# Performance work log

Measured on AMD Instinct MI355X. Metric: run time of the kernel, lower is better.

Reference implementation:

```python
import jax, jax.numpy as jnp
import numpy as np

B, S, H = 16, 384, 768
DK, ESS, WHOLE = 64, 6, 8
HEADER = WHOLE + 1
NL_RGAT = 2


def _sinusoidal_pos(seq_len, dim):
    pos = np.arange(seq_len)[:, None]
    j = np.arange(dim)[None, :]
    enc = pos / np.power(10000.0, 2 * (j // 2) / dim)
    sent = dim // 2
    out = np.zeros((seq_len, dim), dtype=np.float32)
    out[:, :sent] = np.sin(enc[:, 0::2])
    out[:, sent:] = np.cos(enc[:, 1::2])
    return jnp.asarray(out)[None, None]  # [1,1,S,dim]


def _rope(pos, x):
    sin, cos = jnp.split(pos, 2, axis=-1)
    sin_pos = jnp.stack([sin, sin], -1).reshape(pos.shape)
    cos_pos = jnp.stack([cos, cos], -1).reshape(pos.shape)
    rot = jnp.stack([-x[..., 1::2], x[..., 0::2]], -1).reshape(x.shape)
    return x * cos_pos + rot * sin_pos


def _mlp(x, rep_w, rep_b, sc_w, sc_b):
    return jax.nn.relu(x @ rep_w.T + rep_b) @ sc_w.T + sc_b


def _heads(y, mask, n_heads):
    b, s = y.shape[:2]
    return (y * mask).reshape(b, s, n_heads, DK).transpose(0, 2, 1, 3)


def _shaking(M, rows, cols):
    # M: [B,nH,S,S] -> [B,P,nH]; upper triangle (incl diag), row-major
    return M[:, :, rows, cols].transpose(0, 2, 1)


def _layernorm(x, eps=1e-5):
    m = x.mean(-1, keepdims=True)
    v = ((x - m) ** 2).mean(-1, keepdims=True)
    return (x - m) * jax.lax.rsqrt(v + eps)


def setup_inputs() -> dict:
    key = jax.random.key(0)
    ks = jax.random.split(key, 32)
    n = lambda i, shape: jax.random.normal(ks[i], shape, dtype=jnp.float32) * 0.02
    ig = (H + DK * HEADER) // 2          # 672
    ip = (2 * H + DK * ESS) // 2          # 960
    return dict(
        seq_hiddens=jax.random.normal(ks[0], (B, S, H), dtype=jnp.float32),
        attention_mask=jnp.ones((B, S, 1), dtype=jnp.float32),
        wq4gt_w=n(1, (DK, H)), wq4gt_b=n(2, (DK,)),
        wk4gt_w=n(3, (DK, H)), wk4gt_b=n(4, (DK,)),
        wq4g_rep_w=n(5, (ig, H)), wq4g_rep_b=n(6, (ig,)),
        wq4g_sc_w=n(7, (DK * HEADER, ig)), wq4g_sc_b=n(8, (DK * HEADER,)),
        wk4g_rep_w=n(9, (ig, H)), wk4g_rep_b=n(10, (ig,)),
        wk4g_sc_w=n(11, (DK * HEADER, ig)), wk4g_sc_b=n(12, (DK * HEADER,)),
        rgat_w=n(13, (NL_RGAT, HEADER, H, H)),
        wq4t_w=n(14, (DK, 2 * H)), wq4t_b=n(15, (DK,)),
        wk4t_w=n(16, (DK, 2 * H)), wk4t_b=n(17, (DK,)),
        wq_rep_w=n(18, (ip, 2 * H)), wq_rep_b=n(19, (ip,)),
        wq_sc_w=n(20, (DK * ESS, ip)), wq_sc_b=n(21, (DK * ESS,)),
        wk_rep_w=n(22, (ip, 2 * H)), wk_rep_b=n(23, (ip,)),
        wk_sc_w=n(24, (DK * ESS, ip)), wk_sc_b=n(25, (DK * ESS,)),
    )


def reference(seq_hiddens, attention_mask,
              wq4gt_w, wq4gt_b, wk4gt_w, wk4gt_b,
              wq4g_rep_w, wq4g_rep_b, wq4g_sc_w, wq4g_sc_b,
              wk4g_rep_w, wk4g_rep_b, wk4g_sc_w, wk4g_sc_b,
              rgat_w,
              wq4t_w, wq4t_b, wk4t_w, wk4t_b,
              wq_rep_w, wq_rep_b, wq_sc_w, wq_sc_b,
              wk_rep_w, wk_rep_b, wk_sc_w, wk_sc_b):
    pos = _sinusoidal_pos(S, DK)
    rows, cols = np.triu_indices(S)
    inv = 1.0 / np.sqrt(DK).astype(np.float32)
    mask = attention_mask
    x = seq_hiddens

    # ----- graph layer (graph_stack_num = 1) -----
    tsq = _rope(pos, _heads(x @ wq4gt_w.T + wq4gt_b, mask, 1))
    tsk = _rope(pos, _heads(x @ wk4gt_w.T + wk4gt_b, mask, 1))
    thr_g = jax.nn.relu(_shaking(jnp.einsum('bhqd,bhkd->bhqk', tsq, tsk) * inv, rows, cols))

    q = _rope(pos, _heads(_mlp(x, wq4g_rep_w, wq4g_rep_b, wq4g_sc_w, wq4g_sc_b), mask, HEADER))
    k = _rope(pos, _heads(_mlp(x, wk4g_rep_w, wk4g_rep_b, wk4g_sc_w, wk4g_sc_b), mask, HEADER))
    score = jnp.einsum('bhqd,bhkd->bhqk', q, k) * inv  # [B,HEADER,S,S]
    sc_g = _shaking(score[:, :WHOLE], rows, cols)

    upper = jnp.triu(score, 1)
    diag = jnp.triu(score, 0) - upper
    att = upper + jnp.swapaxes(upper, -1, -2) + diag  # symmetric
    adj = jax.nn.softmax(att, -1) * (att != 0)

    feat = x
    for l in range(NL_RGAT):
        hr = jnp.einsum('bsh,roh->brso', feat, rgat_w[l])           # per-relation Linear (no bias)
        agg = jax.nn.relu(jnp.einsum('brst,brto->brso', adj, hr))   # adjacency bmm + ReLU
        feat = _layernorm(jax.nn.relu(agg.sum(1)) / HEADER)         # (dropout is eval-identity)

    # ----- prediction head -----
    inp = jnp.concatenate([seq_hiddens, feat], -1)  # [B,S,2H]
    tq = _rope(pos, _heads(inp @ wq4t_w.T + wq4t_b, mask, 1))
    tk = _rope(pos, _heads(inp @ wk4t_w.T + wk4t_b, mask, 1))
    thr_p = jax.nn.relu(_shaking(jnp.einsum('bhqd,bhkd->bhqk', tq, tk) * inv, rows, cols))

    qp = _rope(pos, _heads(_mlp(inp, wq_rep_w, wq_rep_b, wq_sc_w, wq_sc_b), mask, ESS))
    kp = _rope(pos, _heads(_mlp(inp, wk_rep_w, wk_rep_b, wk_sc_w, wk_sc_b), mask, ESS))
    sc_p = _shaking(jnp.einsum('bhqd,bhkd->bhqk', qp, kp) * inv, rows, cols)

    # concat all shaking outputs along last dim: [B, S(S+1)/2, ESS+1+WHOLE+1]
    return jnp.concatenate([sc_p, thr_p, sc_g, thr_g], -1)
```

## Files before the change

### kernel.cpp

```cpp
#include <hip/hip_runtime.h>
#include <math.h>

typedef unsigned short ushort_t;
typedef __attribute__((ext_vector_type(8))) short short8;
typedef __attribute__((ext_vector_type(4))) float f32x4;

constexpr int B = 16, S = 384, H = 768;
constexpr int BS = B * S;
constexpr long long PAIRS = (long long)S * (S + 1) / 2;
constexpr float INV = 0.125f;

__device__ __forceinline__ ushort_t f2bf(float f) {
  unsigned int u = __float_as_uint(f);
  u += 0x7FFF + ((u >> 16) & 1);
  return (ushort_t)(u >> 16);
}
__device__ __forceinline__ float bf2f(ushort_t u) {
  return __uint_as_float(((unsigned int)u) << 16);
}

__device__ __forceinline__ void glds16(const ushort_t* g, ushort_t* l) {
  __builtin_amdgcn_global_load_lds(
      (const __attribute__((address_space(1))) unsigned int*)g,
      (__attribute__((address_space(3))) unsigned int*)l, 16, 0, 0);
}

__global__ __launch_bounds__(256) void setup_kernel(
    float* tab,
    const float* g_repq, const float* g_repk, const float* g_gtq, const float* g_gtk,
    const float* p_repq, const float* p_repk, const float* p_gtq, const float* p_gtk,
    const float* g_scq, const float* g_sck, const float* p_scq, const float* p_sck,
    float* bqkg, float* bqkp, float* bscg, float* bscp) {
  int b = blockIdx.x;
  if (b < 48) {
    int s = b * 8 + (threadIdx.x >> 5);
    int i = threadIdx.x & 31;
    double ang = (double)s / pow(10000.0, (double)i / 32.0);
    tab[s * 64 + 2 * i]     = (float)cos(ang);
    tab[s * 64 + 2 * i + 1] = (float)sin(ang);
  } else {
    int t = (b - 48) * 256 + threadIdx.x;
    if (t < 1472)
      bqkg[t] = t < 672 ? g_repq[t] : t < 1344 ? g_repk[t - 672]
              : t < 1408 ? g_gtq[t - 1344] : g_gtk[t - 1408];
    if (t < 2048)
      bqkp[t] = t < 960 ? p_repq[t] : t < 1920 ? p_repk[t - 960]
              : t < 1984 ? p_gtq[t - 1920] : p_gtk[t - 1984];
    if (t < 1152) bscg[t] = t < 576 ? g_scq[t] : g_sck[t - 576];
    if (t < 768)  bscp[t] = t < 384 ? p_scq[t] : p_sck[t - 384];
  }
}

constexpr int NJOBS = 14;
struct CvtJobs {
  const float* src[NJOBS];
  ushort_t* dst[NJOBS];
  int n_real[NJOBS];
  int n_tot[NJOBS];
  int blk_off[NJOBS + 1];
};
__global__ __launch_bounds__(256) void cvt_jobs_kernel(CvtJobs J) {
  int blk = blockIdx.x;
  int j = 0;
  while (j < NJOBS - 1 && blk >= J.blk_off[j + 1]) ++j;
  int i4 = (blk - J.blk_off[j]) * 256 + threadIdx.x;
  if (i4 * 4 >= J.n_tot[j]) return;
  ushort4 o;
  if (i4 * 4 < J.n_real[j]) {
    float4 v = ((const float4*)J.src[j])[i4];
    o = make_ushort4(f2bf(v.x), f2bf(v.y), f2bf(v.z), f2bf(v.w));
  } else {
    o = make_ushort4(0, 0, 0, 0);
  }
  ((ushort4*)J.dst[j])[i4] = o;
}

template <int ACT, int CMODE, int SWZ>
__global__ __launch_bounds__(256) void gemm_nt_mfma(
    const ushort_t* __restrict__ A, const ushort_t* __restrict__ W,
    const float* __restrict__ bias, void* __restrict__ Cv,
    ushort_t* __restrict__ pl, ushort_t* __restrict__ qd,
    ushort_t* __restrict__ kd, int cbase, int nsplit,
    int N, int K, int lda, int ldw, int ldc, float alpha, int nh,
    long long sAb, long long sAh, long long sWb, long long sWh,
    long long sCb, long long sCh,
    const float* __restrict__ mask, const float* __restrict__ tab, int biasN) {
  constexpr int SHSZ = (CMODE == 2 || CMODE == 8) ? 17408 : 16384;
  __shared__ __align__(16) ushort_t SH[SHSZ];
  int bx = blockIdx.x, by = blockIdx.y, bz = blockIdx.z;
  if (SWZ) {
    const int nx = gridDim.x, ny = gridDim.y;
    const int nwg = nx * ny * gridDim.z;
    const int hw = bx + nx * (by + ny * bz);
    int l = (hw & 7) * (nwg >> 3) + (hw >> 3);
    const int pz = l / (nx * ny);
    int l2 = l - pz * (nx * ny);
    const int GM = 8;
    const int band = l2 / (GM * nx);
    const int rem = l2 - band * (GM * nx);
    const int gm = (ny - band * GM < GM) ? (ny - band * GM) : GM;
    bx = rem / gm;
    by = band * GM + (rem - bx * gm);
    bz = pz;
  }
  const int zb = bz / nh, zh = bz - zb * nh;
  A += zb * sAb + zh * sAh;
  W += zb * sWb + zh * sWh;
  const int t = threadIdx.x;
  int m0, n0;
  if (CMODE == 3 || CMODE == 8) {
    const int ti = (bx < 3) ? 0 : (bx < 5 ? 1 : 2);
    const int tj = (bx < 3) ? bx : (bx < 5 ? bx - 2 : 2);
    m0 = ti * 128; n0 = tj * 128;
  } else {
    m0 = by * 128; n0 = bx * 128;
  }
  const int lane = t & 63, wid = t >> 6;
  const int wr = wid >> 1, wc = wid & 1;
  const int lrow = lane & 15, lk = lane >> 4;
  const int srow = t >> 2, sch = (t & 3) * 8;
  const ushort_t* Ag = A + (size_t)(m0 + srow) * lda + sch;
  const ushort_t* Wg = W + (size_t)(n0 + srow) * ldw + sch;
  const size_t a64 = (size_t)64 * lda, w64 = (size_t)64 * ldw;

  f32x4 acc[4][4];
#pragma unroll
  for (int i = 0; i < 4; ++i)
#pragma unroll
    for (int j = 0; j < 4; ++j) acc[i][j] = (f32x4){0.f, 0.f, 0.f, 0.f};

  auto stage = [&](int k0, int buf) {
    const int ao = buf * 4096, bo = 8192 + buf * 4096;
    glds16(Ag + k0, &SH[ao + t * 8]);
    glds16(Ag + k0 + a64, &SH[ao + 2048 + t * 8]);
    glds16(Wg + k0, &SH[bo + t * 8]);
    glds16(Wg + k0 + w64, &SH[bo + 2048 + t * 8]);
  };

  const int nk = K >> 5;
  stage(0, 0);
  for (int s = 0; s < nk; ++s) {
    __syncthreads();
    if (s + 1 < nk) stage((s + 1) << 5, (s + 1) & 1);
    const int ao = (s & 1) * 4096, bo = 8192 + (s & 1) * 4096;
    short8 av[4], bv[4];
#pragma unroll
    for (int i = 0; i < 4; ++i) {
      av[i] = *(const short8*)&SH[ao + (wr * 64 + i * 16 + lrow) * 32 + lk * 8];
      bv[i] = *(const short8*)&SH[bo + (wc * 64 + i * 16 + lrow) * 32 + lk * 8];
    }
#pragma unroll
    for (int i = 0; i < 4; ++i)
#pragma unroll
      for (int j = 0; j < 4; ++j)
        acc[i][j] = __builtin_amdgcn_mfma_f32_16x16x32_bf16(av[i], bv[j],
                                                            acc[i][j], 0, 0, 0);
  }

  if (CMODE == 2) {
    __syncthreads();
    const int bb = m0 / S;
    ushort_t* Cb = (ushort_t*)Cv + (size_t)bb * sCb;
    const int s_base = m0 - bb * S;
#pragma unroll
    for (int i = 0; i < 4; ++i) {
      const int sl = wr * 64 + i * 16 + lk * 4;
#pragma unroll
      for (int j = 0; j < 4; ++j) {
        const int nl = wc * 64 + j * 16 + lrow;
        ushort4 o = make_ushort4(f2bf(acc[i][j][0]), f2bf(acc[i][j][1]),
                                 f2bf(acc[i][j][2]), f2bf(acc[i][j][3]));
        *(ushort4*)&SH[nl * 136 + sl] = o;
      }
    }
    __syncthreads();
#pragma unroll
    for (int it = 0; it < 8; ++it) {
      const int row = it * 16 + wid * 4 + lk;
      ushort_t* dst = Cb + (size_t)(n0 + row) * ldc + s_base + lrow * 8;
      *(short8*)dst = *(const short8*)&SH[row * 136 + lrow * 8];
    }
  } else if (CMODE == 3) {
    ushort_t* plc = pl + ((size_t)(cbase + zh) * B + zb) * PAIRS;
#pragma unroll
    for (int j = 0; j < 4; ++j) {
      const int n = n0 + wc * 64 + j * 16 + lrow;
#pragma unroll
      for (int i = 0; i < 4; ++i) {
#pragma unroll
        for (int e = 0; e < 4; ++e) {
          const int m = m0 + wr * 64 + i * 16 + lk * 4 + e;
          if (n >= m) {
            long long p = (long long)m * S - (long long)m * (m - 1) / 2 + (n - m);
            float v = alpha * acc[i][j][e];
            if (ACT == 1) v = fmaxf(v, 0.f);
            plc[p] = f2bf(v);
          }
        }
      }
    }
  } else if (CMODE == 5) {
    ushort_t* Cq = qd + (size_t)zh * sCh;
    const float* bz2 = bias + (size_t)zh * biasN;
#pragma unroll
    for (int j = 0; j < 4; ++j) {
      const int n = n0 + wc * 64 + j * 16 + lrow;
      const float vb = (n < N) ? bz2[n] : 0.f;
      const int d = n & 63;
      const int ti2 = d & ~1;
#pragma unroll
      for (int i = 0; i < 4; ++i) {
#pragma unroll
        for (int e = 0; e < 4; ++e) {
          const int m = m0 + wr * 64 + i * 16 + lk * 4 + e;
          const int s = m % S;
          float v = (n < N) ? (acc[i][j][e] + vb) : 0.f;
          float pv = __shfl_xor(v, 1);
          float c = tab[s * 64 + ti2], sn = tab[s * 64 + ti2 + 1];
          float o = (d & 1) ? (v * c + pv * sn) : (v * c - pv * sn);
          o *= mask[m];
          if (n < N) Cq[(size_t)m * ldc + n] = f2bf(o);
        }
      }
    }
  } else if (CMODE == 6) {
    ushort_t* Cu = (ushort_t*)Cv;
#pragma unroll
    for (int j = 0; j < 4; ++j) {
      const int n = n0 + wc * 64 + j * 16 + lrow;
      const float vb = (n < N) ? bias[n] : 0.f;
#pragma unroll
      for (int i = 0; i < 4; ++i) {
#pragma unroll
        for (int e = 0; e < 4; ++e) {
          const int m = m0 + wr * 64 + i * 16 + lk * 4 + e;
          float v = (n < N) ? (acc[i][j][e] + vb) : 0.f;
          float pv = __shfl_xor(v, 1);
          if (n < nsplit) {
            Cu[(size_t)m * ldc + n] = f2bf(fmaxf(v, 0.f));
          } else if (n < N) {
            const int d = n - nsplit;
            const int dd = d & 63;
            const int ti2 = dd & ~1;
            const int s = m % S;
            float c = tab[s * 64 + ti2], sn = tab[s * 64 + ti2 + 1];
            float o = (dd & 1) ? (v * c + pv * sn) : (v * c - pv * sn);
            o *= mask[m];
            if (d < 64) qd[(size_t)m * 64 + dd] = f2bf(o);
            else        kd[(size_t)m * 64 + dd] = f2bf(o);
          }
        }
      }
    }
  } else if (CMODE == 8) {
    ushort_t* Cu = (ushort_t*)Cv + zb * sCb + zh * sCh;
    ushort_t* plc = pl + ((size_t)(cbase + zh) * B + zb) * PAIRS;
    const bool diag = (m0 == n0);
#pragma unroll
    for (int j = 0; j < 4; ++j) {
      const int n = n0 + wc * 64 + j * 16 + lrow;
#pragma unroll
      for (int i = 0; i < 4; ++i) {
#pragma unroll
        for (int e = 0; e < 4; ++e) {
          const int m = m0 + wr * 64 + i * 16 + lk * 4 + e;
          float v = alpha * acc[i][j][e];
          ushort_t vb = f2bf(v);
          if (!diag || n >= m) Cu[(size_t)m * ldc + n] = vb;
          if (zh < 8 && n >= m) {
            long long p = (long long)m * S - (long long)m * (m - 1) / 2 + (n - m);
            plc[p] = vb;
          }
        }
      }
    }
    __syncthreads();
#pragma unroll
    for (int i = 0; i < 4; ++i) {
      const int sl = wr * 64 + i * 16 + lk * 4;
#pragma unroll
      for (int j = 0; j < 4; ++j) {
        const int nl = wc * 64 + j * 16 + lrow;
        ushort4 o4 = make_ushort4(f2bf(alpha * acc[i][j][0]),
                                  f2bf(alpha * acc[i][j][1]),
                                  f2bf(alpha * acc[i][j][2]),
                                  f2bf(alpha * acc[i][j][3]));
        *(ushort4*)&SH[nl * 136 + sl] = o4;
      }
    }
    __syncthreads();
#pragma unroll
    for (int it = 0; it < 8; ++it) {
      const int rowN = it * 16 + wid * 4 + lk;
      const int colM = lrow * 8;
      if (!diag) {
        *(short8*)&Cu[(size_t)(n0 + rowN) * ldc + m0 + colM] =
            *(const short8*)&SH[rowN * 136 + colM];
      } else {
#pragma unroll
        for (int q = 0; q < 8; ++q)
          if (rowN > colM + q)
            Cu[(size_t)(n0 + rowN) * ldc + m0 + colM + q] =
                SH[rowN * 136 + colM + q];
      }
    }
  }
}

__global__ __launch_bounds__(256) void adj_bmm_kernel(
    const ushort_t* __restrict__ adjb, const ushort_t* __restrict__ hrt,
    float* __restrict__ P0, float* __restrict__ P1, float* __restrict__ P2) {
  __shared__ __align__(16) ushort_t As[2][128 * 32];
  __shared__ __align__(16) ushort_t Bs[2][128 * 32];
  int bx = blockIdx.x, by = blockIdx.y, bz = blockIdx.z;
  {
    int nx = gridDim.x, ny = gridDim.y;
    int nwg = nx * ny * gridDim.z;
    int flat = bx + nx * (by + ny * bz);
    int l = (flat & 7) * (nwg >> 3) + (flat >> 3);
    bx = l % nx; l /= nx; by = l % ny; bz = l / ny;
  }
  const int b = bz / 3, rg = bz - b * 3;
  float* P = (rg == 0) ? P0 : (rg == 1) ? P1 : P2;
  const int t = threadIdx.x;
  const int m0 = by * 128, n0 = bx * 128;
  const int lane = t & 63, wid = t >> 6;
  const int wr = wid >> 1, wc = wid & 1;
  const int lrow = lane & 15, lk = lane >> 4;
  const int srow = t >> 2, sch = (t & 3) * 8;

  const ushort_t* adjA =
      adjb + ((size_t)(b * 9 + rg * 3) * S + m0 + srow) * S + sch;
  const ushort_t* hrA =
      hrt + ((size_t)(b * 9 + rg * 3) * H + n0 + srow) * S + sch;

  float mac[4][4][4];
#pragma unroll
  for (int i = 0; i < 4; ++i)
#pragma unroll
    for (int j = 0; j < 4; ++j)
#pragma unroll
      for (int e = 0; e < 4; ++e) mac[i][j][e] = 0.f;

  f32x4 acc[4][4];
#pragma unroll
  for (int i = 0; i < 4; ++i)
#pragma unroll
    for (int j = 0; j < 4; ++j) acc[i][j] = (f32x4){0.f, 0.f, 0.f, 0.f};

  auto stage = [&](int s, int buf) {
    const int rr = s / 12;
    const int k0 = (s - rr * 12) * 32;
    const ushort_t* Ag = adjA + (size_t)rr * S * S + k0;
    const ushort_t* Wg = hrA + (size_t)rr * H * S + k0;
    glds16(Ag, &As[buf][t * 8]);
    glds16(Ag + 64 * S, &As[buf][2048 + t * 8]);
    glds16(Wg, &Bs[buf][t * 8]);
    glds16(Wg + 64 * S, &Bs[buf][2048 + t * 8]);
  };

  stage(0, 0);
  for (int s = 0; s < 36; ++s) {
    __syncthreads();
    if (s + 1 < 36) stage(s + 1, (s + 1) & 1);
    const int buf = s & 1;
    short8 av[4], bv[4];
#pragma unroll
    for (int i = 0; i < 4; ++i) {
      av[i] = *(const short8*)&As[buf][(wr * 64 + i * 16 + lrow) * 32 + lk * 8];
      bv[i] = *(const short8*)&Bs[buf][(wc * 64 + i * 16 + lrow) * 32 + lk * 8];
    }
#pragma unroll
    for (int i = 0; i < 4; ++i)
#pragma unroll
      for (int j = 0; j < 4; ++j)
        acc[i][j] = __builtin_amdgcn_mfma_f32_16x16x32_bf16(av[i], bv[j],
                                                            acc[i][j], 0, 0, 0);
    if ((s % 12) == 11) {
#pragma unroll
      for (int i = 0; i < 4; ++i)
#pragma unroll
        for (int j = 0; j < 4; ++j) {
#pragma unroll
          for (int e = 0; e < 4; ++e)
            mac[i][j][e] += fmaxf(acc[i][j][e], 0.f);
          acc[i][j] = (f32x4){0.f, 0.f, 0.f, 0.f};
        }
    }
  }

#pragma unroll
  for (int i = 0; i < 4; ++i)
#pragma unroll
    for (int j = 0; j < 4; ++j)
#pragma unroll
      for (int e = 0; e < 4; ++e) {
        const int m = m0 + wr * 64 + i * 16 + lk * 4 + e;
        const int n = n0 + wc * 64 + j * 16 + lrow;
        P[((size_t)b * S + m) * H + n] = mac[i][j][e];
      }
}

__global__ __launch_bounds__(128) void softmax_mask_kernel(
    const ushort_t* __restrict__ Mt, ushort_t* __restrict__ adjb) {
  __shared__ float red[128];
  int row = blockIdx.x;
  const ushort_t* r = Mt + (size_t)row * S;
  ushort_t* o = adjb + (size_t)row * S;
  int t = threadIdx.x;
  const bool act = t < 96;
  float v[4];
  float mx = -INFINITY;
  if (act) {
    ushort4 u = ((const ushort4*)r)[t];
    v[0] = bf2f(u.x); v[1] = bf2f(u.y); v[2] = bf2f(u.z); v[3] = bf2f(u.w);
    mx = fmaxf(fmaxf(v[0], v[1]), fmaxf(v[2], v[3]));
  }
  red[t] = mx; __syncthreads();
  for (int off2 = 64; off2 > 0; off2 >>= 1) {
    if (t < off2) red[t] = fmaxf(red[t], red[t + off2]);
    __syncthreads();
  }
  mx = red[0]; __syncthreads();
  float e4[4], s = 0.f;
  if (act) {
#pragma unroll
    for (int q = 0; q < 4; ++q) { e4[q] = expf(v[q] - mx); s += e4[q]; }
  }
  red[t] = s; __syncthreads();
  for (int off2 = 64; off2 > 0; off2 >>= 1) {
    if (t < off2) red[t] += red[t + off2];
    __syncthreads();
  }
  float invs = 1.f / red[0];
  if (act) {
    ushort4 ou;
    ou.x = f2bf((v[0] != 0.f) ? e4[0] * invs : 0.f);
    ou.y = f2bf((v[1] != 0.f) ? e4[1] * invs : 0.f);
    ou.z = f2bf((v[2] != 0.f) ? e4[2] * invs : 0.f);
    ou.w = f2bf((v[3] != 0.f) ? e4[3] * invs : 0.f);
    ((ushort4*)o)[t] = ou;
  }
}

__global__ __launch_bounds__(256) void ln_finalize_kernel(
    const float* __restrict__ P0, const float* __restrict__ P1,
    const float* __restrict__ P2, const ushort_t* __restrict__ xb,
    ushort_t* __restrict__ inp) {
  __shared__ float red[256];
  int row = blockIdx.x;
  const size_t base = (size_t)row * H;
  ushort_t* xrow = inp + (size_t)row * (2 * H);
  ushort_t* fb = xrow + H;
  int t = threadIdx.x;
  float v[3];
  float s = 0.f;
#pragma unroll
  for (int q = 0; q < 3; ++q) {
    size_t ix = base + t + q * 256;
    v[q] = (P0[ix] + P1[ix] + P2[ix]) / 9.0f;
    s += v[q];
  }
  red[t] = s; __syncthreads();
#pragma unroll
  for (int q = 0; q < 3; ++q)
    xrow[t + q * 256] = xb[base + t + q * 256];
  for (int off2 = 128; off2 > 0; off2 >>= 1) {
    if (t < off2) red[t] += red[t + off2];
    __syncthreads();
  }
  float mean = red[0] / (float)H; __syncthreads();
  float s2 = 0.f;
#pragma unroll
  for (int q = 0; q < 3; ++q) { float d = v[q] - mean; s2 += d * d; }
  red[t] = s2; __syncthreads();
  for (int off2 = 128; off2 > 0; off2 >>= 1) {
    if (t < off2) red[t] += red[t + off2];
    __syncthreads();
  }
  float var = red[0] / (float)H;
  float rs = rsqrtf(var + 1e-5f);
#pragma unroll
  for (int q = 0; q < 3; ++q)
    fb[t + q * 256] = f2bf((v[q] - mean) * rs);
}

__global__ __launch_bounds__(256) void gather16_kernel(
    const ushort_t* __restrict__ plA, const ushort_t* __restrict__ plB,
    float* __restrict__ out) {
  int idx = blockIdx.x * 256 + threadIdx.x;
  if (idx >= (int)(B * PAIRS)) return;
  const size_t PLN = (size_t)B * PAIRS;
  float v[16];
#pragma unroll
  for (int ch = 0; ch < 7; ++ch)  v[ch] = bf2f(plA[(size_t)ch * PLN + idx]);
#pragma unroll
  for (int ch = 7; ch < 16; ++ch) v[ch] = bf2f(plB[(size_t)(ch - 7) * PLN + idx]);
  float4* dst = (float4*)(out + (size_t)idx * 16);
#pragma unroll
  for (int q = 0; q < 4; ++q)
    dst[q] = make_float4(v[4 * q], v[4 * q + 1], v[4 * q + 2], v[4 * q + 3]);
}

extern "C" void kernel_launch(void* const* d_in, const int* in_sizes, int n_in,
                              void* d_out, int out_size, void* d_ws, size_t ws_size,
                              hipStream_t stream) {
  (void)in_sizes; (void)n_in; (void)out_size; (void)ws_size;
  const float* x          = (const float*)d_in[0];
  const float* mask       = (const float*)d_in[1];
  const float* wq4gt_w    = (const float*)d_in[2];
  const float* wq4gt_b    = (const float*)d_in[3];
  const float* wk4gt_w    = (const float*)d_in[4];
  const float* wk4gt_b    = (const float*)d_in[5];
  const float* wq4g_rep_w = (const float*)d_in[6];
  const float* wq4g_rep_b = (const float*)d_in[7];
  const float* wq4g_sc_w  = (const float*)d_in[8];
  const float* wq4g_sc_b  = (const float*)d_in[9];
  const float* wk4g_rep_w = (const float*)d_in[10];
  const float* wk4g_rep_b = (const float*)d_in[11];
  const float* wk4g_sc_w  = (const float*)d_in[12];
  const float* wk4g_sc_b  = (const float*)d_in[13];
  const float* rgat_w     = (const float*)d_in[14];
  const float* wq4t_w     = (const float*)d_in[15];
  const float* wq4t_b     = (const float*)d_in[16];
  const float* wk4t_w     = (const float*)d_in[17];
  const float* wk4t_b     = (const float*)d_in[18];
  const float* wq_rep_w   = (const float*)d_in[19];
  const float* wq_rep_b   = (const float*)d_in[20];
  const float* wq_sc_w    = (const float*)d_in[21];
  const float* wq_sc_b    = (const float*)d_in[22];
  const float* wk_rep_w   = (const float*)d_in[23];
  const float* wk_rep_b   = (const float*)d_in[24];
  const float* wk_sc_w    = (const float*)d_in[25];
  const float* wk_sc_b    = (const float*)d_in[26];
  float* out = (float*)d_out;

  char* wsb = (char*)d_ws;
  size_t off = 0;
  auto af = [&](size_t n) { float* p = (float*)(wsb + off);
                            off += ((n * 4 + 255) & ~(size_t)255); return p; };
  auto au = [&](size_t n) { ushort_t* p = (ushort_t*)(wsb + off);
                            off += ((n * 2 + 255) & ~(size_t)255); return p; };

  float* t_rope = af(24576);
  float* t_scg  = af((size_t)B * 9 * S * S);
  float* t_acc  = af((size_t)BS * H);
  ushort_t* xb    = au((size_t)BS * H);
  ushort_t* inpb  = au((size_t)BS * 2 * H);
  ushort_t* repb  = au((size_t)BS * 1920);
  ushort_t* qb    = au((size_t)BS * 576);
  ushort_t* kb    = au((size_t)BS * 576);
  ushort_t* adjb  = au((size_t)B * 9 * S * S);
  ushort_t* plB   = au((size_t)9 * B * PAIRS);
  ushort_t* wqkg  = au(1179648);
  ushort_t* wqkp  = au(3145728);
  ushort_t* wq4g_scb = au(430080);
  ushort_t* wk4g_scb = au(430080);
  ushort_t* wq_scb   = au(368640);
  ushort_t* wk_scb   = au(368640);
  ushort_t* rgatb    = au(10616832);
  float* bqkg = af(1472);
  float* bqkp = af(2048);
  float* bscg = af(1152);
  float* bscp = af(768);

  ushort_t* scg_u = (ushort_t*)t_scg;
  ushort_t* hr_t  = (ushort_t*)t_scg;
  ushort_t* plA   = rgatb;
  float* P0 = t_acc;
  float* P1 = (float*)repb;
  float* P2 = (float*)inpb;

  setup_kernel<<<56, 256, 0, stream>>>(
      t_rope,
      wq4g_rep_b, wk4g_rep_b, wq4gt_b, wk4gt_b,
      wq_rep_b, wk_rep_b, wq4t_b, wk4t_b,
      wq4g_sc_b, wk4g_sc_b, wq_sc_b, wk_sc_b,
      bqkg, bqkp, bscg, bscp);

  {
    CvtJobs J;
    const float* srcs[NJOBS] = {wq4g_rep_w, wk4g_rep_w, wq4gt_w, wk4gt_w,
                                wq_rep_w, wk_rep_w, wq4t_w, wk4t_w,
                                wq4g_sc_w, wk4g_sc_w, wq_sc_w, wk_sc_w,
                                rgat_w, x};
    ushort_t* dsts[NJOBS] = {wqkg, wqkg + 516096, wqkg + 1032192, wqkg + 1081344,
                             wqkp, wqkp + 1474560, wqkp + 2949120, wqkp + 3047424,
                             wq4g_scb, wk4g_scb, wq_scb, wk_scb,
                             rgatb, xb};
    int nreal[NJOBS] = {516096, 516096, 49152, 49152,
                        1474560, 1474560, 98304, 98304,
                        387072, 387072, 368640, 368640,
                        10616832, 4718592};
    int ntot[NJOBS]  = {516096, 516096, 49152, 98304,
                        1474560, 1474560, 98304, 98304,
                        430080, 430080, 368640, 368640,
                        10616832, 4718592};
    int acc_blk = 0;
    for (int j = 0; j < NJOBS; ++j) {
      J.src[j] = srcs[j]; J.dst[j] = dsts[j];
      J.n_real[j] = nreal[j]; J.n_tot[j] = ntot[j];
      J.blk_off[j] = acc_blk;
      acc_blk += (ntot[j] + 1023) / 1024;
    }
    J.blk_off[NJOBS] = acc_blk;
    cvt_jobs_kernel<<<acc_blk, 256, 0, stream>>>(J);
  }

  gemm_nt_mfma<0, 6, 1><<<dim3(12, 48, 1), 256, 0, stream>>>(
      xb, wqkg, bqkg, repb, nullptr, qb, kb, 0, 1344,
      1472, 768, 768, 768, 1344, 1.f, 1, 0, 0, 0, 0, 0, 0,
      mask, t_rope, 0);
  gemm_nt_mfma<1, 3, 1><<<dim3(6, 1, B), 256, 0, stream>>>(
      qb, kb, nullptr, nullptr, plB, nullptr, nullptr, 8, 0,
      S, 64, 64, 64, 0, INV, 1,
      (long long)S * 64, 0, (long long)S * 64, 0, 0, 0,
      nullptr, nullptr, 0);

  gemm_nt_mfma<0, 5, 1><<<dim3(5, 48, 2), 256, 0, stream>>>(
      repb, wq4g_scb, bscg, nullptr, nullptr, qb, nullptr, 0, 0,
      576, 672, 1344, 672, 576, 1.f, 2,
      0, 672, 0, 430080, 0, (long long)BS * 576,
      mask, t_rope, 576);
  gemm_nt_mfma<0, 8, 1><<<dim3(6, 1, B * 9), 256, 0, stream>>>(
      qb, kb, nullptr, scg_u, plB, nullptr, nullptr, 0, 0,
      S, 64, 576, 576, S, INV, 9,
      (long long)S * 576, 64, (long long)S * 576, 64,
      (long long)9 * S * S, (long long)S * S,
      nullptr, nullptr, 0);
  softmax_mask_kernel<<<B * 9 * S, 128, 0, stream>>>(scg_u, adjb);

  for (int l = 0; l < 2; ++l) {
    const ushort_t* fsrc = (l == 0) ? xb : inpb + H;
    const int flda = (l == 0) ? H : 2 * H;
    gemm_nt_mfma<0, 2, 1><<<dim3(54, 48, 1), 256, 0, stream>>>(
        fsrc, rgatb + (size_t)l * 9 * H * H, nullptr, hr_t, nullptr, nullptr,
        nullptr, 0, 0,
        9 * H, H, flda, H, S, 1.f, 1, 0, 0, 0, 0, (long long)9 * H * S, 0,
        nullptr, nullptr, 0);
    adj_bmm_kernel<<<dim3(6, 3, B * 3), 256, 0, stream>>>(adjb, hr_t, P0, P1, P2);
    ln_finalize_kernel<<<BS, 256, 0, stream>>>(P0, P1, P2, xb, inpb);
  }

  gemm_nt_mfma<0, 6, 1><<<dim3(16, 48, 1), 256, 0, stream>>>(
      inpb, wqkp, bqkp, repb, nullptr, qb, kb, 0, 1920,
      2048, 1536, 1536, 1536, 1920, 1.f, 1, 0, 0, 0, 0, 0, 0,
      mask, t_rope, 0);
  gemm_nt_mfma<1, 3, 1><<<dim3(6, 1, B), 256, 0, stream>>>(
      qb, kb, nullptr, nullptr, plA, nullptr, nullptr, 6, 0,
      S, 64, 64, 64, 0, INV, 1,
      (long long)S * 64, 0, (long long)S * 64, 0, 0, 0,
      nullptr, nullptr, 0);

  gemm_nt_mfma<0, 5, 1><<<dim3(3, 48, 2), 256, 0, stream>>>(
      repb, wq_scb, bscp, nullptr, nullptr, qb, nullptr, 0, 0,
      384, 960, 1920, 960, 384, 1.f, 2,
      0, 960, 0, 368640, 0, (long long)BS * 384,
      mask, t_rope, 384);
  gemm_nt_mfma<0, 3, 1><<<dim3(6, 1, B * 6), 256, 0, stream>>>(
      qb, qb + (size_t)BS * 384, nullptr, nullptr, plA, nullptr, nullptr, 0, 0,
      S, 64, 384, 384, 0, INV, 6,
      (long long)S * 384, 64, (long long)S * 384, 64, 0, 0,
      nullptr, nullptr, 0);

  gather16_kernel<<<(int)((B * PAIRS + 255) / 256), 256, 0, stream>>>(plA, plB, out);
}
```

Baseline: 652.8 us.

## Split adjacency bmm into five relation groups with bf16 partial outputs

The adjacency-bmm kernel now splits the 9 relations into 5 groups (four of two relations, one of one) instead of 3 groups of three. This raises the grid from 864 to 1440 workgroups for better occupancy. Partial sums are now stored as bf16 rather than fp32, so the write and read traffic stays modest even with more partial buffers. The cost is imbalanced work per block (24 vs 12 steps), bf16 rounding on the partials before the layernorm, and reuse of the qb and repb scratch buffers as partial storage.

```diff
diff --git a/kernel.cpp b/kernel.cpp
--- a/kernel.cpp
+++ b/kernel.cpp
@@ -309,7 +309,9 @@
 
 __global__ __launch_bounds__(256) void adj_bmm_kernel(
     const ushort_t* __restrict__ adjb, const ushort_t* __restrict__ hrt,
-    float* __restrict__ P0, float* __restrict__ P1, float* __restrict__ P2) {
+    ushort_t* __restrict__ Q0, ushort_t* __restrict__ Q1,
+    ushort_t* __restrict__ Q2, ushort_t* __restrict__ Q3,
+    ushort_t* __restrict__ Q4) {
   __shared__ __align__(16) ushort_t As[2][128 * 32];
   __shared__ __align__(16) ushort_t Bs[2][128 * 32];
   int bx = blockIdx.x, by = blockIdx.y, bz = blockIdx.z;
@@ -320,8 +322,11 @@
     int l = (flat & 7) * (nwg >> 3) + (flat >> 3);
     bx = l % nx; l /= nx; by = l % ny; bz = l / ny;
   }
-  const int b = bz / 3, rg = bz - b * 3;
-  float* P = (rg == 0) ? P0 : (rg == 1) ? P1 : P2;
+  const int b = bz / 5, rg = bz - b * 5;
+  ushort_t* Q = (rg == 0) ? Q0 : (rg == 1) ? Q1 : (rg == 2) ? Q2
+              : (rg == 3) ? Q3 : Q4;
+  const int rel0 = (rg < 4) ? rg * 2 : 8;
+  const int nsteps = (rg < 4) ? 24 : 12;
   const int t = threadIdx.x;
   const int m0 = by * 128, n0 = bx * 128;
   const int lane = t & 63, wid = t >> 6;
@@ -330,9 +335,9 @@
   const int srow = t >> 2, sch = (t & 3) * 8;
 
   const ushort_t* adjA =
-      adjb + ((size_t)(b * 9 + rg * 3) * S + m0 + srow) * S + sch;
+      adjb + ((size_t)(b * 9 + rel0) * S + m0 + srow) * S + sch;
   const ushort_t* hrA =
-      hrt + ((size_t)(b * 9 + rg * 3) * H + n0 + srow) * S + sch;
+      hrt + ((size_t)(b * 9 + rel0) * H + n0 + srow) * S + sch;
 
   float mac[4][4][4];
 #pragma unroll
@@ -360,9 +365,9 @@
   };
 
   stage(0, 0);
-  for (int s = 0; s < 36; ++s) {
-    __syncthreads();
-    if (s + 1 < 36) stage(s + 1, (s + 1) & 1);
+  for (int s = 0; s < nsteps; ++s) {
+    __syncthreads();
+    if (s + 1 < nsteps) stage(s + 1, (s + 1) & 1);
     const int buf = s & 1;
     short8 av[4], bv[4];
 #pragma unroll
@@ -397,7 +402,7 @@
       for (int e = 0; e < 4; ++e) {
         const int m = m0 + wr * 64 + i * 16 + lk * 4 + e;
         const int n = n0 + wc * 64 + j * 16 + lrow;
-        P[((size_t)b * S + m) * H + n] = mac[i][j][e];
+        Q[((size_t)b * S + m) * H + n] = f2bf(mac[i][j][e]);
       }
 }
 
@@ -444,8 +449,9 @@
 }
 
 __global__ __launch_bounds__(256) void ln_finalize_kernel(
-    const float* __restrict__ P0, const float* __restrict__ P1,
-    const float* __restrict__ P2, const ushort_t* __restrict__ xb,
+    const ushort_t* __restrict__ Q0, const ushort_t* __restrict__ Q1,
+    const ushort_t* __restrict__ Q2, const ushort_t* __restrict__ Q3,
+    const ushort_t* __restrict__ Q4, const ushort_t* __restrict__ xb,
     ushort_t* __restrict__ inp) {
   __shared__ float red[256];
   int row = blockIdx.x;
@@ -458,7 +464,8 @@
 #pragma unroll
   for (int q = 0; q < 3; ++q) {
     size_t ix = base + t + q * 256;
-    v[q] = (P0[ix] + P1[ix] + P2[ix]) / 9.0f;
+    v[q] = (bf2f(Q0[ix]) + bf2f(Q1[ix]) + bf2f(Q2[ix]) + bf2f(Q3[ix]) +
+            bf2f(Q4[ix])) / 9.0f;
     s += v[q];
   }
   red[t] = s; __syncthreads();
@@ -567,9 +574,11 @@
   ushort_t* scg_u = (ushort_t*)t_scg;
   ushort_t* hr_t  = (ushort_t*)t_scg;
   ushort_t* plA   = rgatb;
-  float* P0 = t_acc;
-  float* P1 = (float*)repb;
-  float* P2 = (float*)inpb;
+  ushort_t* Q0 = (ushort_t*)t_acc;
+  ushort_t* Q1 = Q0 + (size_t)BS * H;
+  ushort_t* Q2 = repb;
+  ushort_t* Q3 = Q2 + (size_t)BS * H;
+  ushort_t* Q4 = qb;
 
   setup_kernel<<<56, 256, 0, stream>>>(
       t_rope,
@@ -638,8 +647,9 @@
         nullptr, 0, 0,
         9 * H, H, flda, H, S, 1.f, 1, 0, 0, 0, 0, (long long)9 * H * S, 0,
         nullptr, nullptr, 0);
-    adj_bmm_kernel<<<dim3(6, 3, B * 3), 256, 0, stream>>>(adjb, hr_t, P0, P1, P2);
-    ln_finalize_kernel<<<BS, 256, 0, stream>>>(P0, P1, P2, xb, inpb);
+    adj_bmm_kernel<<<dim3(6, 3, B * 5), 256, 0, stream>>>(
+        adjb, hr_t, Q0, Q1, Q2, Q3, Q4);
+    ln_finalize_kernel<<<BS, 256, 0, stream>>>(Q0, Q1, Q2, Q3, Q4, xb, inpb);
   }
 
   gemm_nt_mfma<0, 6, 1><<<dim3(16, 48, 1), 256, 0, stream>>>(
```

Result: no change. 654.0 us (+0.2%).
